# Optimization experiments

Measured on AMD Instinct MI355X. Metric: run time of the kernel, lower is better.

## Reference

```python
import jax, jax.numpy as jnp
import numpy as np

B, S, D, H = 2, 2048, 64, 12  # batch, seq, richness (per-head dim), heads
NEG = -99999.0


def setup_inputs() -> dict:
    key = jax.random.key(0)
    ks = jax.random.split(key, 9)
    s_in = 1.0 / np.sqrt(D)
    s_out = 1.0 / np.sqrt(H * D)
    return {
        "x": jax.random.normal(ks[0], (B, S, D), dtype=jnp.float32),
        "Wq": jax.random.uniform(ks[1], (D, H * D), jnp.float32, -s_in, s_in),
        "bq": jax.random.uniform(ks[2], (H * D,), jnp.float32, -s_in, s_in),
        "Wk": jax.random.uniform(ks[3], (D, H * D), jnp.float32, -s_in, s_in),
        "bk": jax.random.uniform(ks[4], (H * D,), jnp.float32, -s_in, s_in),
        "Wv": jax.random.uniform(ks[5], (D, H * D), jnp.float32, -s_in, s_in),
        "bv": jax.random.uniform(ks[6], (H * D,), jnp.float32, -s_in, s_in),
        "Wo": jax.random.uniform(ks[7], (H * D, D), jnp.float32, -s_out, s_out),
        "bo": jax.random.uniform(ks[8], (D,), jnp.float32, -s_out, s_out),
    }


def reference(x, Wq, bq, Wk, bk, Wv, bv, Wo, bo):
    b, s, d = x.shape
    def split_heads(y):
        return y.reshape(b, s, H, d).transpose(0, 2, 1, 3)  # [B,H,S,D]
    q = split_heads(x @ Wq + bq)
    k = split_heads(x @ Wk + bk)
    v = split_heads(x @ Wv + bv)
    # NOTE: no 1/sqrt(d) scaling, faithful to original module.
    scores = jnp.einsum("bhqd,bhkd->bhqk", q, k)  # [B,H,S,S]
    # Faithful quirky mask: tril of the scores, then mask where it's zero.
    mask = jnp.tril(scores)
    scores = jnp.where(mask == 0, NEG, scores)
    p = jax.nn.softmax(scores, axis=-1)
    o = jnp.einsum("bhqk,bhkd->bhqd", p, v)  # [B,H,S,D]
    o = o.transpose(0, 2, 1, 3).reshape(b, s, H * d)
    return o @ Wo + bo
```

## Files before the change

kernel.cpp:

```cpp
#include <hip/hip_runtime.h>
#include <math.h>

#define BB 2
#define SS 2048
#define DD 64
#define HH 12
#define CFIX 16.0f

typedef _Float16 v8h __attribute__((ext_vector_type(8)));
typedef short    v8s __attribute__((ext_vector_type(8)));
typedef float    v4f __attribute__((ext_vector_type(4)));
typedef unsigned int v2u __attribute__((ext_vector_type(2)));

__device__ __forceinline__ unsigned short f2bf(float f) {
    unsigned u = __float_as_uint(f);
    u += 0x7FFF + ((u >> 16) & 1);
    return (unsigned short)(u >> 16);
}

__device__ __forceinline__ void async16(const void* g, void* l) {
    __builtin_amdgcn_global_load_lds(
        (const __attribute__((address_space(1))) unsigned int*)g,
        (__attribute__((address_space(3))) unsigned int*)l, 16, 0, 0);
}

__global__ __launch_bounds__(256) void qkv_kernel(
    const float* __restrict__ x,
    const float* __restrict__ Wq, const float* __restrict__ bq,
    const float* __restrict__ Wk, const float* __restrict__ bk,
    const float* __restrict__ Wv, const float* __restrict__ bv,
    const float* __restrict__ Wo, _Float16* __restrict__ WoT,
    _Float16* __restrict__ Q16, _Float16* __restrict__ K16,
    unsigned short* __restrict__ VT)
{
    __shared__ float xs[16 * 64];
    const int rBase = blockIdx.x * 16;
    const int cg    = blockIdx.y;
    const int mat   = cg / 3;
    const int col   = (cg % 3) * 256 + threadIdx.x;

    if (cg == 0 && blockIdx.x < 192) {
        int e = blockIdx.x * 256 + threadIdx.x;
        int k = e >> 6, c2 = e & 63;
        WoT[c2 * 768 + k] = (_Float16)Wo[e];
    }

    const float* W    = (mat == 0) ? Wq : (mat == 1) ? Wk : Wv;
    const float* bias = (mat == 0) ? bq : (mat == 1) ? bk : bv;

    for (int i = threadIdx.x; i < 16 * 64; i += 256)
        xs[i] = x[rBase * 64 + i];
    __syncthreads();

    float acc[16];
#pragma unroll
    for (int r = 0; r < 16; r++) acc[r] = 0.f;

    for (int k = 0; k < 64; k++) {
        float w = W[k * 768 + col];
#pragma unroll
        for (int r = 0; r < 16; r++) acc[r] += xs[r * 64 + k] * w;
    }

    const float bb = bias[col];
    const int h = col >> 6, d = col & 63;

    if (mat < 2) {
        _Float16* Out = (mat == 0) ? Q16 : K16;
#pragma unroll
        for (int r = 0; r < 16; r++) {
            int row = rBase + r;
            int b = row >> 11, s = row & 2047;
            Out[(((size_t)b * HH + h) * SS + s) * 64 + d] = (_Float16)(acc[r] + bb);
        }
    } else {
        const int b = rBase >> 11, s0 = rBase & 2047;
        unsigned short tmp[16];
#pragma unroll
        for (int r = 0; r < 16; r++) tmp[r] = f2bf(acc[r] + bb);
        size_t base = ((size_t)(b * HH + h) * 64 + d) * SS + s0;
        v8s w0, w1;
#pragma unroll
        for (int r = 0; r < 8; r++) { w0[r] = (short)tmp[r]; w1[r] = (short)tmp[r + 8]; }
        *(v8s*)&VT[base]     = w0;
        *(v8s*)&VT[base + 8] = w1;
    }
}

__global__ __launch_bounds__(256, 4) void attn_kernel(
    const _Float16* __restrict__ Q16, const _Float16* __restrict__ K16,
    const unsigned short* __restrict__ VTg, _Float16* __restrict__ O16)
{
    __shared__ __align__(16) _Float16       Kl[2][64 * 64];
    __shared__ __align__(16) unsigned short Vl[2][64 * 64];
    __shared__ __align__(16) unsigned short Pl[4][16 * 40];

    const int bh    = blockIdx.y;
    const int qtile = (int)((blockIdx.x + 11 * blockIdx.y) & 63);
    const int qBase = qtile * 32;
    const int wave  = threadIdx.x >> 6;
    const int lane  = threadIdx.x & 63;
    const int llow  = lane & 15;
    const int quad  = lane >> 4;
    const int rowg  = wave & 1;
    const int keyh  = wave >> 1;
    const int q0    = qBase + rowg * 16;

    const _Float16*       Kp = K16 + (size_t)bh * SS * 64;
    const unsigned short* Vp = VTg + (size_t)bh * 64 * SS;

    const _Float16* Qp = Q16 + ((size_t)bh * SS + q0) * 64;
    v8h qa0 = *(const v8h*)(Qp + llow * 64 + quad * 8);
    v8h qa1 = *(const v8h*)(Qp + llow * 64 + 32 + quad * 8);

    v4f o[4];
    float lacc = 0.f;
#pragma unroll
    for (int nb = 0; nb < 4; nb++) o[nb] = (v4f){0.f, 0.f, 0.f, 0.f};

    const int nt = qtile / 2 + 1;

#pragma unroll
    for (int rep = 0; rep < 2; rep++) {
        int c = rep * 256 + threadIdx.x;
        int row = c >> 3, g = (c & 7) ^ (row & 7);
        async16(Kp + (size_t)row * 64 + g * 8, &Kl[0][(rep * 256 + wave * 64) * 8]);
        async16(Vp + (size_t)row * SS + g * 8, &Vl[0][(rep * 256 + wave * 64) * 8]);
    }

    for (int t = 0; t < nt; t++) {
        __syncthreads();
        if (t + 1 < nt) {
            const int ktn = (t + 1) * 64, bufn = (t + 1) & 1;
#pragma unroll
            for (int rep = 0; rep < 2; rep++) {
                int c = rep * 256 + threadIdx.x;
                int row = c >> 3, g = (c & 7) ^ (row & 7);
                async16(Kp + (size_t)(ktn + row) * 64 + g * 8,
                        &Kl[bufn][(rep * 256 + wave * 64) * 8]);
                async16(Vp + (size_t)row * SS + ktn + g * 8,
                        &Vl[bufn][(rep * 256 + wave * 64) * 8]);
            }
        }
        const int buf = t & 1, kt = t * 64;
        const int sw = llow & 7;

        v4f sc[2];
#pragma unroll
        for (int cb = 0; cb < 2; cb++) {
            const int rk = 32 * keyh + 16 * cb + llow;
            v8h k0 = *(const v8h*)&Kl[buf][rk * 64 + ((quad ^ sw)) * 8];
            v8h k1 = *(const v8h*)&Kl[buf][rk * 64 + (((4 + quad) ^ sw)) * 8];
            v4f a = (v4f){0.f, 0.f, 0.f, 0.f};
            a = __builtin_amdgcn_mfma_f32_16x16x32_f16(k0, qa0, a, 0, 0, 0);
            a = __builtin_amdgcn_mfma_f32_16x16x32_f16(k1, qa1, a, 0, 0, 0);
            sc[cb] = a;
        }

        const int qrow = q0 + llow;
#pragma unroll
        for (int cb = 0; cb < 2; cb++) {
            const int kbase = kt + 32 * keyh + 16 * cb + quad * 4;
            unsigned dw[2];
#pragma unroll
            for (int h2 = 0; h2 < 2; h2++) {
                unsigned lo, hi;
#pragma unroll
                for (int j = 0; j < 2; j++) {
                    const int r = h2 * 2 + j;
                    const float sv = sc[cb][r];
                    const float e  = __expf(sv - CFIX);
                    const float p  = (kbase + r <= qrow && sv != 0.f) ? e : 0.f;
                    lacc += p;
                    if (j == 0) lo = __float_as_uint(p);
                    else        hi = __float_as_uint(p);
                }
                dw[h2] = (lo >> 16) | (hi & 0xFFFF0000u);
            }
            *(v2u*)&Pl[wave][llow * 40 + 16 * cb + 4 * quad] = (v2u){dw[0], dw[1]};
        }

        v8s pa = *(const v8s*)&Pl[wave][llow * 40 + quad * 8];

#pragma unroll
        for (int nb = 0; nb < 4; nb++) {
            const int rv = 16 * nb + llow;
            v8s vv = *(const v8s*)&Vl[buf][rv * 64 + (((4 * keyh + quad) ^ sw)) * 8];
            o[nb] = __builtin_amdgcn_mfma_f32_16x16x32_bf16(pa, vv, o[nb], 0, 0, 0);
        }
    }

    lacc += __shfl_xor(lacc, 16);
    lacc += __shfl_xor(lacc, 32);

    __syncthreads();
    float* redO = (float*)&Kl[0][0];
    float* redL = (float*)&Vl[0][0];
    if (keyh == 1) {
#pragma unroll
        for (int nb = 0; nb < 4; nb++)
#pragma unroll
            for (int r = 0; r < 4; r++)
                redO[(rowg * 16 + quad * 4 + r) * 68 + 16 * nb + llow] = o[nb][r];
        if (lane < 16)
            redL[rowg * 16 + lane] = lacc;
    }
    __syncthreads();
    if (keyh == 0) {
        float lr[4];
#pragma unroll
        for (int r = 0; r < 4; r++)
            lr[r] = __shfl(lacc, quad * 4 + r) + redL[rowg * 16 + quad * 4 + r];
        _Float16* Op = O16 + ((size_t)bh * SS + q0) * 64;
#pragma unroll
        for (int nb = 0; nb < 4; nb++)
#pragma unroll
            for (int r = 0; r < 4; r++) {
                float v = o[nb][r] + redO[(rowg * 16 + quad * 4 + r) * 68 + 16 * nb + llow];
                Op[(quad * 4 + r) * 64 + 16 * nb + llow] = (_Float16)(v / lr[r]);
            }
    }
}

__global__ __launch_bounds__(256) void out_kernel(
    const _Float16* __restrict__ O16, const _Float16* __restrict__ WoT,
    const float* __restrict__ bo, float* __restrict__ out)
{
    __shared__ __align__(16) float red[4][16][66];
    const int r0   = blockIdx.x * 16;
    const int wave = threadIdx.x >> 6, lane = threadIdx.x & 63;
    const int llow = lane & 15, quad = lane >> 4;
    const int b = r0 >> 11, s = r0 & 2047;

    v4f acc[4];
#pragma unroll
    for (int cb = 0; cb < 4; cb++) acc[cb] = (v4f){0.f, 0.f, 0.f, 0.f};

#pragma unroll
    for (int i = 0; i < 6; i++) {
        const int kb = wave * 6 + i;
        const int h = kb >> 1, dseg = (kb & 1) * 32;
        v8h af = *(const v8h*)(O16 + ((size_t)(b * HH + h) * SS + s + llow) * 64 + dseg + quad * 8);
#pragma unroll
        for (int cb = 0; cb < 4; cb++) {
            v8h bf = *(const v8h*)(WoT + (size_t)(16 * cb + llow) * 768 + kb * 32 + quad * 8);
            acc[cb] = __builtin_amdgcn_mfma_f32_16x16x32_f16(af, bf, acc[cb], 0, 0, 0);
        }
    }

#pragma unroll
    for (int cb = 0; cb < 4; cb++)
#pragma unroll
        for (int r = 0; r < 4; r++)
            red[wave][quad * 4 + r][16 * cb + llow] = acc[cb][r];
    __syncthreads();

    const int col = threadIdx.x & 63, rr = threadIdx.x >> 6;
    const float bias = bo[col];
    for (int i = rr; i < 16; i += 4) {
        float sum = red[0][i][col] + red[1][i][col] + red[2][i][col] + red[3][i][col] + bias;
        out[(size_t)(r0 + i) * 64 + col] = sum;
    }
}

extern "C" void kernel_launch(void* const* d_in, const int* in_sizes, int n_in,
                              void* d_out, int out_size, void* d_ws, size_t ws_size,
                              hipStream_t stream)
{
    const float* x  = (const float*)d_in[0];
    const float* Wq = (const float*)d_in[1];
    const float* bq = (const float*)d_in[2];
    const float* Wk = (const float*)d_in[3];
    const float* bk = (const float*)d_in[4];
    const float* Wv = (const float*)d_in[5];
    const float* bv = (const float*)d_in[6];
    const float* Wo = (const float*)d_in[7];
    const float* bo = (const float*)d_in[8];
    float* out = (float*)d_out;

    char* w = (char*)d_ws;
    const size_t MB6 = (size_t)BB * HH * SS * DD * 2;
    _Float16*       Q16 = (_Float16*)(w);
    _Float16*       K16 = (_Float16*)(w + MB6);
    unsigned short* VT  = (unsigned short*)(w + 2 * MB6);
    _Float16*       O16 = (_Float16*)(w + 3 * MB6);
    _Float16*       WoT = (_Float16*)(w + 4 * MB6);

    qkv_kernel<<<dim3(256, 9), 256, 0, stream>>>(x, Wq, bq, Wk, bk, Wv, bv, Wo, WoT, Q16, K16, VT);
    attn_kernel<<<dim3(64, BB * HH), 256, 0, stream>>>(Q16, K16, VT, O16);
    out_kernel<<<(BB * SS) / 16, 256, 0, stream>>>(O16, WoT, bo, out);
}
```

Baseline: 155.8 us.

## Use MFMA for QKV projection and load K/V directly into registers in attention

```diff
diff --git a/kernel.cpp b/kernel.cpp
--- a/kernel.cpp
+++ b/kernel.cpp
@@ -18,82 +18,96 @@
     return (unsigned short)(u >> 16);
 }
 
-__device__ __forceinline__ void async16(const void* g, void* l) {
-    __builtin_amdgcn_global_load_lds(
-        (const __attribute__((address_space(1))) unsigned int*)g,
-        (__attribute__((address_space(3))) unsigned int*)l, 16, 0, 0);
+__global__ __launch_bounds__(256) void prep_kernel(
+    const float* __restrict__ x,
+    const float* __restrict__ Wq, const float* __restrict__ Wk,
+    const float* __restrict__ Wv, const float* __restrict__ Wo,
+    _Float16* __restrict__ x16, _Float16* __restrict__ W16,
+    _Float16* __restrict__ WoT)
+{
+    const int idx = blockIdx.x * 256 + threadIdx.x;
+    if (idx < 262144) {
+        x16[idx] = (_Float16)x[idx];
+    } else if (idx < 262144 + 147456) {
+        const int t = idx - 262144;
+        const int k = t / 2304, c = t % 2304;
+        const int mat = c / 768, cc = c % 768;
+        const float* W = (mat == 0) ? Wq : (mat == 1) ? Wk : Wv;
+        W16[c * 64 + k] = (_Float16)W[k * 768 + cc];
+    } else {
+        const int e = idx - 262144 - 147456;
+        WoT[(e & 63) * 768 + (e >> 6)] = (_Float16)Wo[e];
+    }
 }
 
 __global__ __launch_bounds__(256) void qkv_kernel(
-    const float* __restrict__ x,
-    const float* __restrict__ Wq, const float* __restrict__ bq,
-    const float* __restrict__ Wk, const float* __restrict__ bk,
-    const float* __restrict__ Wv, const float* __restrict__ bv,
-    const float* __restrict__ Wo, _Float16* __restrict__ WoT,
+    const _Float16* __restrict__ x16, const _Float16* __restrict__ W16,
+    const float* __restrict__ bq, const float* __restrict__ bk,
+    const float* __restrict__ bv,
     _Float16* __restrict__ Q16, _Float16* __restrict__ K16,
     unsigned short* __restrict__ VT)
 {
-    __shared__ float xs[16 * 64];
-    const int rBase = blockIdx.x * 16;
-    const int cg    = blockIdx.y;
-    const int mat   = cg / 3;
-    const int col   = (cg % 3) * 256 + threadIdx.x;
-
-    if (cg == 0 && blockIdx.x < 192) {
-        int e = blockIdx.x * 256 + threadIdx.x;
-        int k = e >> 6, c2 = e & 63;
-        WoT[c2 * 768 + k] = (_Float16)Wo[e];
-    }
-
-    const float* W    = (mat == 0) ? Wq : (mat == 1) ? Wk : Wv;
+    const int r0  = blockIdx.x * 64;
+    const int c0g = blockIdx.y * 64;
+    const int mat = c0g / 768, cc0 = c0g % 768;
+    const int h   = cc0 >> 6;
+    const int b   = r0 >> 11, s0 = r0 & 2047;
+
+    const int wave = threadIdx.x >> 6, lane = threadIdx.x & 63;
+    const int llow = lane & 15, quad = lane >> 4;
+    const int rowbase = r0 + 16 * wave;
+
     const float* bias = (mat == 0) ? bq : (mat == 1) ? bk : bv;
 
-    for (int i = threadIdx.x; i < 16 * 64; i += 256)
-        xs[i] = x[rBase * 64 + i];
-    __syncthreads();
-
-    float acc[16];
-#pragma unroll
-    for (int r = 0; r < 16; r++) acc[r] = 0.f;
-
-    for (int k = 0; k < 64; k++) {
-        float w = W[k * 768 + col];
-#pragma unroll
-        for (int r = 0; r < 16; r++) acc[r] += xs[r * 64 + k] * w;
-    }
-
-    const float bb = bias[col];
-    const int h = col >> 6, d = col & 63;
-
+    v8h a0 = *(const v8h*)(x16 + (size_t)(rowbase + llow) * 64 + quad * 8);
+    v8h a1 = *(const v8h*)(x16 + (size_t)(rowbase + llow) * 64 + 32 + quad * 8);
+
+    v4f acc[4];
+    float bv4[4];
+#pragma unroll
+    for (int nb = 0; nb < 4; nb++) {
+        const int col = c0g + 16 * nb + llow;
+        v8h b0 = *(const v8h*)(W16 + (size_t)col * 64 + quad * 8);
+        v8h b1 = *(const v8h*)(W16 + (size_t)col * 64 + 32 + quad * 8);
+        v4f a = (v4f){0.f, 0.f, 0.f, 0.f};
+        a = __builtin_amdgcn_mfma_f32_16x16x32_f16(a0, b0, a, 0, 0, 0);
+        a = __builtin_amdgcn_mfma_f32_16x16x32_f16(a1, b1, a, 0, 0, 0);
+        acc[nb] = a;
+        bv4[nb] = bias[cc0 + 16 * nb + llow];
+    }
+
+    const int bh = b * HH + h;
     if (mat < 2) {
         _Float16* Out = (mat == 0) ? Q16 : K16;
 #pragma unroll
-        for (int r = 0; r < 16; r++) {
-            int row = rBase + r;
-            int b = row >> 11, s = row & 2047;
-            Out[(((size_t)b * HH + h) * SS + s) * 64 + d] = (_Float16)(acc[r] + bb);
-        }
+        for (int nb = 0; nb < 4; nb++)
+#pragma unroll
+            for (int r = 0; r < 4; r++) {
+                const int s = s0 + 16 * wave + quad * 4 + r;
+                Out[((size_t)bh * SS + s) * 64 + 16 * nb + llow] =
+                    (_Float16)(acc[nb][r] + bv4[nb]);
+            }
     } else {
-        const int b = rBase >> 11, s0 = rBase & 2047;
-        unsigned short tmp[16];
-#pragma unroll
-        for (int r = 0; r < 16; r++) tmp[r] = f2bf(acc[r] + bb);
-        size_t base = ((size_t)(b * HH + h) * 64 + d) * SS + s0;
-        v8s w0, w1;
-#pragma unroll
-        for (int r = 0; r < 8; r++) { w0[r] = (short)tmp[r]; w1[r] = (short)tmp[r + 8]; }
-        *(v8s*)&VT[base]     = w0;
-        *(v8s*)&VT[base + 8] = w1;
-    }
-}
-
-__global__ __launch_bounds__(256, 4) void attn_kernel(
+#pragma unroll
+        for (int nb = 0; nb < 4; nb++) {
+            const int d = 16 * nb + llow;
+            const int s = s0 + 16 * wave + quad * 4;
+            unsigned short p0 = f2bf(acc[nb][0] + bv4[nb]);
+            unsigned short p1 = f2bf(acc[nb][1] + bv4[nb]);
+            unsigned short p2 = f2bf(acc[nb][2] + bv4[nb]);
+            unsigned short p3 = f2bf(acc[nb][3] + bv4[nb]);
+            v2u pk = (v2u){(unsigned)p0 | ((unsigned)p1 << 16),
+                           (unsigned)p2 | ((unsigned)p3 << 16)};
+            *(v2u*)&VT[((size_t)bh * 64 + d) * SS + s] = pk;
+        }
+    }
+}
+
+__global__ __launch_bounds__(128, 4) void attn_kernel(
     const _Float16* __restrict__ Q16, const _Float16* __restrict__ K16,
     const unsigned short* __restrict__ VTg, _Float16* __restrict__ O16)
 {
-    __shared__ __align__(16) _Float16       Kl[2][64 * 64];
-    __shared__ __align__(16) unsigned short Vl[2][64 * 64];
-    __shared__ __align__(16) unsigned short Pl[4][16 * 40];
+    __shared__ __align__(16) unsigned short Pl[2][16 * 72];
 
     const int bh    = blockIdx.y;
     const int qtile = (int)((blockIdx.x + 11 * blockIdx.y) & 63);
@@ -102,9 +116,7 @@
     const int lane  = threadIdx.x & 63;
     const int llow  = lane & 15;
     const int quad  = lane >> 4;
-    const int rowg  = wave & 1;
-    const int keyh  = wave >> 1;
-    const int q0    = qBase + rowg * 16;
+    const int q0    = qBase + 16 * wave;
 
     const _Float16*       Kp = K16 + (size_t)bh * SS * 64;
     const unsigned short* Vp = VTg + (size_t)bh * 64 * SS;
@@ -119,52 +131,42 @@
     for (int nb = 0; nb < 4; nb++) o[nb] = (v4f){0.f, 0.f, 0.f, 0.f};
 
     const int nt = qtile / 2 + 1;
-
-#pragma unroll
-    for (int rep = 0; rep < 2; rep++) {
-        int c = rep * 256 + threadIdx.x;
-        int row = c >> 3, g = (c & 7) ^ (row & 7);
-        async16(Kp + (size_t)row * 64 + g * 8, &Kl[0][(rep * 256 + wave * 64) * 8]);
-        async16(Vp + (size_t)row * SS + g * 8, &Vl[0][(rep * 256 + wave * 64) * 8]);
-    }
+    const int qrow = q0 + llow;
 
     for (int t = 0; t < nt; t++) {
-        __syncthreads();
-        if (t + 1 < nt) {
-            const int ktn = (t + 1) * 64, bufn = (t + 1) & 1;
-#pragma unroll
-            for (int rep = 0; rep < 2; rep++) {
-                int c = rep * 256 + threadIdx.x;
-                int row = c >> 3, g = (c & 7) ^ (row & 7);
-                async16(Kp + (size_t)(ktn + row) * 64 + g * 8,
-                        &Kl[bufn][(rep * 256 + wave * 64) * 8]);
-                async16(Vp + (size_t)row * SS + ktn + g * 8,
-                        &Vl[bufn][(rep * 256 + wave * 64) * 8]);
-            }
-        }
-        const int buf = t & 1, kt = t * 64;
-        const int sw = llow & 7;
-
-        v4f sc[2];
-#pragma unroll
-        for (int cb = 0; cb < 2; cb++) {
-            const int rk = 32 * keyh + 16 * cb + llow;
-            v8h k0 = *(const v8h*)&Kl[buf][rk * 64 + ((quad ^ sw)) * 8];
-            v8h k1 = *(const v8h*)&Kl[buf][rk * 64 + (((4 + quad) ^ sw)) * 8];
+        const int kt = t * 64;
+
+        v8h ka[4][2];
+#pragma unroll
+        for (int cb = 0; cb < 4; cb++) {
+            const _Float16* kr = Kp + (size_t)(kt + 16 * cb + llow) * 64 + quad * 8;
+            ka[cb][0] = *(const v8h*)kr;
+            ka[cb][1] = *(const v8h*)(kr + 32);
+        }
+        v8s va[4][2];
+#pragma unroll
+        for (int nb = 0; nb < 4; nb++) {
+            const unsigned short* vr = Vp + (size_t)(16 * nb + llow) * SS + kt + quad * 8;
+            va[nb][0] = *(const v8s*)vr;
+            va[nb][1] = *(const v8s*)(vr + 32);
+        }
+
+        v4f sc[4];
+#pragma unroll
+        for (int cb = 0; cb < 4; cb++) {
             v4f a = (v4f){0.f, 0.f, 0.f, 0.f};
-            a = __builtin_amdgcn_mfma_f32_16x16x32_f16(k0, qa0, a, 0, 0, 0);
-            a = __builtin_amdgcn_mfma_f32_16x16x32_f16(k1, qa1, a, 0, 0, 0);
+            a = __builtin_amdgcn_mfma_f32_16x16x32_f16(ka[cb][0], qa0, a, 0, 0, 0);
+            a = __builtin_amdgcn_mfma_f32_16x16x32_f16(ka[cb][1], qa1, a, 0, 0, 0);
             sc[cb] = a;
         }
 
-        const int qrow = q0 + llow;
-#pragma unroll
-        for (int cb = 0; cb < 2; cb++) {
-            const int kbase = kt + 32 * keyh + 16 * cb + quad * 4;
+#pragma unroll
+        for (int cb = 0; cb < 4; cb++) {
+            const int kbase = kt + 16 * cb + quad * 4;
             unsigned dw[2];
 #pragma unroll
             for (int h2 = 0; h2 < 2; h2++) {
-                unsigned lo, hi;
+                unsigned lo = 0, hi = 0;
 #pragma unroll
                 for (int j = 0; j < 2; j++) {
                     const int r = h2 * 2 + j;
@@ -177,49 +179,31 @@
                 }
                 dw[h2] = (lo >> 16) | (hi & 0xFFFF0000u);
             }
-            *(v2u*)&Pl[wave][llow * 40 + 16 * cb + 4 * quad] = (v2u){dw[0], dw[1]};
-        }
-
-        v8s pa = *(const v8s*)&Pl[wave][llow * 40 + quad * 8];
+            *(v2u*)&Pl[wave][llow * 72 + 16 * cb + 4 * quad] = (v2u){dw[0], dw[1]};
+        }
+
+        v8s pa0 = *(const v8s*)&Pl[wave][llow * 72 + quad * 8];
+        v8s pa1 = *(const v8s*)&Pl[wave][llow * 72 + 32 + quad * 8];
 
 #pragma unroll
         for (int nb = 0; nb < 4; nb++) {
-            const int rv = 16 * nb + llow;
-            v8s vv = *(const v8s*)&Vl[buf][rv * 64 + (((4 * keyh + quad) ^ sw)) * 8];
-            o[nb] = __builtin_amdgcn_mfma_f32_16x16x32_bf16(pa, vv, o[nb], 0, 0, 0);
+            o[nb] = __builtin_amdgcn_mfma_f32_16x16x32_bf16(pa0, va[nb][0], o[nb], 0, 0, 0);
+            o[nb] = __builtin_amdgcn_mfma_f32_16x16x32_bf16(pa1, va[nb][1], o[nb], 0, 0, 0);
         }
     }
 
     lacc += __shfl_xor(lacc, 16);
     lacc += __shfl_xor(lacc, 32);
-
-    __syncthreads();
-    float* redO = (float*)&Kl[0][0];
-    float* redL = (float*)&Vl[0][0];
-    if (keyh == 1) {
-#pragma unroll
-        for (int nb = 0; nb < 4; nb++)
-#pragma unroll
-            for (int r = 0; r < 4; r++)
-                redO[(rowg * 16 + quad * 4 + r) * 68 + 16 * nb + llow] = o[nb][r];
-        if (lane < 16)
-            redL[rowg * 16 + lane] = lacc;
-    }
-    __syncthreads();
-    if (keyh == 0) {
-        float lr[4];
+    float lr[4];
+#pragma unroll
+    for (int r = 0; r < 4; r++)
+        lr[r] = __shfl(lacc, quad * 4 + r);
+    _Float16* Op = O16 + ((size_t)bh * SS + q0) * 64;
+#pragma unroll
+    for (int nb = 0; nb < 4; nb++)
 #pragma unroll
         for (int r = 0; r < 4; r++)
-            lr[r] = __shfl(lacc, quad * 4 + r) + redL[rowg * 16 + quad * 4 + r];
-        _Float16* Op = O16 + ((size_t)bh * SS + q0) * 64;
-#pragma unroll
-        for (int nb = 0; nb < 4; nb++)
-#pragma unroll
-            for (int r = 0; r < 4; r++) {
-                float v = o[nb][r] + redO[(rowg * 16 + quad * 4 + r) * 68 + 16 * nb + llow];
-                Op[(quad * 4 + r) * 64 + 16 * nb + llow] = (_Float16)(v / lr[r]);
-            }
-    }
+            Op[(quad * 4 + r) * 64 + 16 * nb + llow] = (_Float16)(o[nb][r] / lr[r]);
 }
 
 __global__ __launch_bounds__(256) void out_kernel(
@@ -279,14 +263,17 @@
     float* out = (float*)d_out;
 
     char* w = (char*)d_ws;
-    const size_t MB6 = (size_t)BB * HH * SS * DD * 2;
-    _Float16*       Q16 = (_Float16*)(w);
-    _Float16*       K16 = (_Float16*)(w + MB6);
-    unsigned short* VT  = (unsigned short*)(w + 2 * MB6);
-    _Float16*       O16 = (_Float16*)(w + 3 * MB6);
-    _Float16*       WoT = (_Float16*)(w + 4 * MB6);
-
-    qkv_kernel<<<dim3(256, 9), 256, 0, stream>>>(x, Wq, bq, Wk, bk, Wv, bv, Wo, WoT, Q16, K16, VT);
-    attn_kernel<<<dim3(64, BB * HH), 256, 0, stream>>>(Q16, K16, VT, O16);
+    const size_t MB = 1024 * 1024;
+    _Float16*       x16 = (_Float16*)(w);
+    _Float16*       W16 = (_Float16*)(w + 512 * 1024);
+    _Float16*       WoT = (_Float16*)(w + 832 * 1024);
+    _Float16*       Q16 = (_Float16*)(w + 1 * MB);
+    _Float16*       K16 = (_Float16*)(w + 7 * MB);
+    unsigned short* VT  = (unsigned short*)(w + 13 * MB);
+    _Float16*       O16 = (_Float16*)(w + 19 * MB);
+
+    prep_kernel<<<1792, 256, 0, stream>>>(x, Wq, Wk, Wv, Wo, x16, W16, WoT);
+    qkv_kernel<<<dim3(64, 36), 256, 0, stream>>>(x16, W16, bq, bk, bv, Q16, K16, VT);
+    attn_kernel<<<dim3(64, BB * HH), 128, 0, stream>>>(Q16, K16, VT, O16);
     out_kernel<<<(BB * SS) / 16, 256, 0, stream>>>(O16, WoT, bo, out);
 }
```

After: 214.4 us. 37.6% more time.
